# Performance work log

Measured on AMD Instinct MI355X. Metric: run time of the kernel, lower is better.

## Reference

```python
import jax, jax.numpy as jnp
import numpy as np

# constants mirroring init_kwargs
SPATIAL_STRIDE = 4
RADIUS2 = 0.5 ** 2
K = 32


def _fps(xyz, m):
    """Iterative farthest point sampling. xyz: [N,3] -> idx [m] int32 (starts at index 0, like pointnet2)."""
    n = xyz.shape[0]

    def body(i, carry):
        dist, idx = carry
        cur = xyz[idx[i]]                              # [3]
        d = jnp.sum((xyz - cur) ** 2, axis=-1)          # [N]
        dist = jnp.minimum(dist, d)
        idx = idx.at[i + 1].set(jnp.argmax(dist).astype(jnp.int32))
        return dist, idx

    dist0 = jnp.full((n,), 1e10, xyz.dtype)
    idx0 = jnp.zeros((m,), jnp.int32)
    _, idx = jax.lax.fori_loop(0, m - 1, body, (dist0, idx0))
    return idx


def setup_inputs() -> dict:
    key = jax.random.key(0)
    ks = jax.random.split(key, 5)
    B, T, N, C = 4, 8, 2048, 64
    C_IN = 2 * C + 3  # grouped feat2 + anchor feat1 + xyz displacement
    xyzs = jax.random.uniform(ks[0], (B, T, N, 3), dtype=jnp.float32)
    features = jax.random.normal(ks[1], (B, T, N, C), dtype=jnp.float32)
    w1 = jax.random.normal(ks[2], (C_IN, 128), dtype=jnp.float32) / np.sqrt(C_IN)
    w2 = jax.random.normal(ks[3], (128, 128), dtype=jnp.float32) / np.sqrt(128)
    w3 = jax.random.normal(ks[4], (128, 256), dtype=jnp.float32) / np.sqrt(128)
    return {
        "xyzs": xyzs, "features": features,
        "w1": w1, "b1": jnp.zeros((128,), jnp.float32),
        "w2": w2, "b2": jnp.zeros((128,), jnp.float32),
        "w3": w3, "b3": jnp.zeros((256,), jnp.float32),
    }


def reference(xyzs, features, w1, b1, w2, b2, w3, b3):
    B, T, N, _ = xyzs.shape
    M = N // SPATIAL_STRIDE

    # temporal replicate padding [1,1]
    xp = jnp.concatenate([xyzs[:, :1], xyzs, xyzs[:, -1:]], axis=1)        # [B,T+2,N,3]
    fp = jnp.concatenate([features[:, :1], features, features[:, -1:]], axis=1)
    # frames processed: i = 1..T (stride 1); neighbor frame = i+1
    xyz_a, xyz_n = xp[:, 1:T + 1], xp[:, 2:T + 2]                          # [B,T,N,3]
    feat_a, feat_n = fp[:, 1:T + 1], fp[:, 2:T + 2]                        # [B,T,N,C]

    gather = jax.vmap(jax.vmap(lambda a, i: a[i]))  # over (B, T)

    # FPS on each anchor frame
    idx = jax.vmap(jax.vmap(lambda p: _fps(p, M)))(xyz_a)                  # [B,T,M]
    anchor = gather(xyz_a, idx)                                            # [B,T,M,3]
    f1 = gather(feat_a, idx)                                               # [B,T,M,C]

    # knn of anchors into next frame, with ball-query radius clamp
    d = jnp.sum((anchor[:, :, :, None, :] - xyz_n[:, :, None, :, :]) ** 2, axis=-1)  # [B,T,M,N]
    negd, idxk = jax.lax.top_k(-d, K)                                      # [B,T,M,K]
    idxk = jnp.where(-negd <= RADIUS2, idxk, idxk[..., :1])                # duplicate nearest outside radius

    gxyz = gather(xyz_n, idxk)                                             # [B,T,M,K,3]
    gf2 = gather(feat_n, idxk)                                             # [B,T,M,K,C]
    disp = gxyz - anchor[:, :, :, None, :]
    h = jnp.concatenate(
        [gf2, jnp.broadcast_to(f1[:, :, :, None, :], gf2.shape), disp], axis=-1)  # [B,T,M,K,2C+3]

    h = jax.nn.relu(h @ w1 + b1)
    h = jax.nn.relu(h @ w2 + b2)
    h = jax.nn.relu(h @ w3 + b3)
    new_features = jnp.max(h, axis=3)                                      # [B,T,M,256]
    return anchor, new_features
```

## Files before the change

### kernel.cpp

```cpp
#include <hip/hip_runtime.h>

#define BB 4
#define TT 8
#define NN 2048
#define CC 64
#define MM 512
#define KK 32
#define H3DIM 256
#define RAD2 0.25f
#define FINF 3.4e38f

typedef _Float16 f16x8 __attribute__((ext_vector_type(8)));
typedef _Float16 f16x4 __attribute__((ext_vector_type(4)));
typedef float f32x4 __attribute__((ext_vector_type(4)));

template <int CTRL>
__device__ __forceinline__ float dpp_max_step(float x) {
    int xi = __builtin_bit_cast(int, x);
    int yi = __builtin_amdgcn_update_dpp(xi, xi, CTRL, 0xf, 0xf, false);
    return fmaxf(x, __builtin_bit_cast(float, yi));
}
__device__ __forceinline__ float wave_max64(float x) {
    x = dpp_max_step<0x111>(x);
    x = dpp_max_step<0x112>(x);
    x = dpp_max_step<0x114>(x);
    x = dpp_max_step<0x118>(x);
    x = dpp_max_step<0x142>(x);
    x = dpp_max_step<0x143>(x);
    return __builtin_bit_cast(float, __builtin_amdgcn_readlane(__builtin_bit_cast(int, x), 63));
}
template <int CTRL>
__device__ __forceinline__ unsigned long long dpp_minkey_step(unsigned long long k) {
    int lo = (int)(unsigned)k;
    int hi = (int)(unsigned)(k >> 32);
    int slo = __builtin_amdgcn_update_dpp(lo, lo, CTRL, 0xf, 0xf, false);
    int shi = __builtin_amdgcn_update_dpp(hi, hi, CTRL, 0xf, 0xf, false);
    unsigned long long s = ((unsigned long long)(unsigned)shi << 32) | (unsigned)slo;
    return s < k ? s : k;
}
__device__ __forceinline__ unsigned long long wave_minkey(unsigned long long k) {
    k = dpp_minkey_step<0x111>(k);
    k = dpp_minkey_step<0x112>(k);
    k = dpp_minkey_step<0x114>(k);
    k = dpp_minkey_step<0x118>(k);
    k = dpp_minkey_step<0x142>(k);
    k = dpp_minkey_step<0x143>(k);
    int lo = __builtin_amdgcn_readlane((int)(unsigned)k, 63);
    int hi = __builtin_amdgcn_readlane((int)(unsigned)(k >> 32), 63);
    return ((unsigned long long)(unsigned)hi << 32) | (unsigned)lo;
}

#define FPP_LDS 52224

__global__ __launch_bounds__(256) void k_fps_pp(const float* __restrict__ xyzs,
                                                const float* __restrict__ feats,
                                                const float* __restrict__ w1,
                                                int* __restrict__ fps_idx,
                                                _Float16* __restrict__ Pp) {
    extern __shared__ char fsm[];
    int tid = threadIdx.x;

    if (blockIdx.x < BB * TT) {
        float* sx = (float*)fsm;
        float* sy = sx + NN;
        float* sz = sy + NN;
        float* pd = sz + NN;
        int* pi = (int*)(pd + 8);
        int bt = blockIdx.x;
        int lane = tid & 63, w = tid >> 6;
        const float* src = xyzs + (size_t)bt * NN * 3;
        for (int i = tid; i < NN; i += 256) {
            sx[i] = src[i * 3 + 0];
            sy[i] = src[i * 3 + 1];
            sz[i] = src[i * 3 + 2];
        }
        __syncthreads();

        float px[8], py[8], pz[8], dist[8];
#pragma unroll
        for (int j = 0; j < 8; ++j) {
            int p = tid * 8 + j;
            px[j] = sx[p]; py[j] = sy[p]; pz[j] = sz[p];
            dist[j] = 1e10f;
        }

        int cur = 0;
        if (tid == 0) fps_idx[bt * MM + 0] = 0;
        int pbase = tid * 8;

        for (int it = 1; it < MM; ++it) {
            float cx = sx[cur], cy = sy[cur], cz = sz[cur];
            float bestd = -1.0f;
            int bestp = 0;
#pragma unroll
            for (int j = 0; j < 8; ++j) {
                float dx = px[j] - cx, dy = py[j] - cy, dz = pz[j] - cz;
                float d = dx * dx + dy * dy + dz * dz;
                float nd = fminf(dist[j], d);
                dist[j] = nd;
                if (nd > bestd) { bestd = nd; bestp = pbase + j; }
            }
            float wmax = wave_max64(bestd);
            unsigned long long mask = __ballot(bestd == wmax);
            int wl = __ffsll(mask) - 1;
            int wbp = __builtin_amdgcn_readlane(bestp, wl);
            if (lane == 0) { pd[(it & 1) * 4 + w] = wmax; pi[(it & 1) * 4 + w] = wbp; }
            __syncthreads();
            float bd = pd[(it & 1) * 4 + 0];
            int bp = pi[(it & 1) * 4 + 0];
#pragma unroll
            for (int q = 1; q < 4; ++q) {
                float d2 = pd[(it & 1) * 4 + q];
                int p2 = pi[(it & 1) * 4 + q];
                if (d2 > bd) { bd = d2; bp = p2; }
            }
            cur = bp;
            if (tid == 0) fps_idx[bt * MM + it] = cur;
        }
    } else {
        float* sw = (float*)fsm;
        float* sin_ = sw + 68 * 128;
        for (int i = tid; i < 68 * 128; i += 256) {
            int r = i >> 7, c = i & 127;
            float v = 0.f;
            if (r < 64) v = w1[r * 128 + c];
            else if (r < 67) v = w1[(128 + r - 64) * 128 + c];
            sw[i] = v;
        }
        int row0 = (blockIdx.x - BB * TT) * 64;
        int bt = row0 >> 11;
        int b = bt >> 3, t = bt & 7;
        int tn = (t + 1 < TT) ? (t + 1) : (TT - 1);
        size_t nbase = (size_t)(b * TT + tn) * NN + (row0 & (NN - 1));
        const float* fsrc = feats + nbase * CC;
        const float* xsrc = xyzs + nbase * 3;
        for (int i = tid; i < 1024; i += 256) {
            float4 v = ((const float4*)fsrc)[i];
            int r = i >> 4, c = (i & 15) * 4;
            *(float4*)&sin_[r * 68 + c] = v;
        }
        if (tid < 192) {
            int r = tid / 3, c = tid - r * 3;
            sin_[r * 68 + 64 + c] = xsrc[tid];
        }
        if (tid < 64) sin_[tid * 68 + 67] = 0.f;
        __syncthreads();

        int rowg = tid >> 5, colg = tid & 31;
        float4 acc[8];
#pragma unroll
        for (int i = 0; i < 8; ++i) acc[i] = make_float4(0.f, 0.f, 0.f, 0.f);
        for (int k = 0; k < 68; k += 4) {
            float4 a4[8], b4[4];
#pragma unroll
            for (int i = 0; i < 8; ++i) a4[i] = *(const float4*)&sin_[(rowg * 8 + i) * 68 + k];
#pragma unroll
            for (int kk = 0; kk < 4; ++kk) b4[kk] = *(const float4*)&sw[(k + kk) * 128 + colg * 4];
#pragma unroll
            for (int i = 0; i < 8; ++i) {
#pragma unroll
                for (int kk = 0; kk < 4; ++kk) {
                    float av = (kk == 0) ? a4[i].x : (kk == 1) ? a4[i].y : (kk == 2) ? a4[i].z : a4[i].w;
                    acc[i].x += av * b4[kk].x;
                    acc[i].y += av * b4[kk].y;
                    acc[i].z += av * b4[kk].z;
                    acc[i].w += av * b4[kk].w;
                }
            }
        }
#pragma unroll
        for (int i = 0; i < 8; ++i) {
            f16x4 h;
            h[0] = (_Float16)acc[i].x; h[1] = (_Float16)acc[i].y;
            h[2] = (_Float16)acc[i].z; h[3] = (_Float16)acc[i].w;
            *(f16x4*)&Pp[(size_t)(row0 + rowg * 8 + i) * 128 + colg * 4] = h;
        }
    }
}

__global__ __launch_bounds__(256) void k_knn(const float* __restrict__ xyzs,
                                             const int* __restrict__ fps_idx,
                                             int* __restrict__ idxk) {
    __shared__ float sx[NN], sy[NN], sz[NN];
    int tid = threadIdx.x;
    int wave = tid >> 6, lane = tid & 63;
    int bt = blockIdx.x >> 6;
    int sub = blockIdx.x & 63;
    int b = bt >> 3, t = bt & 7;
    int tn = (t + 1 < TT) ? (t + 1) : (TT - 1);
    const float* src = xyzs + ((size_t)(b * TT + tn)) * NN * 3;
    for (int i = tid; i < NN; i += 256) {
        sx[i] = src[i * 3 + 0];
        sy[i] = src[i * 3 + 1];
        sz[i] = src[i * 3 + 2];
    }
    __syncthreads();

    for (int a = 0; a < 2; ++a) {
        int mrow = bt * MM + sub * 8 + wave * 2 + a;
        int aidx = fps_idx[mrow];
        const float* xs = xyzs + ((size_t)bt * NN + aidx) * 3;
        float ax = xs[0], ay = xs[1], az = xs[2];
        float d[32];
#pragma unroll
        for (int j = 0; j < 32; ++j) {
            int p = j * 64 + lane;
            float dx = sx[p] - ax, dy = sy[p] - ay, dz = sz[p] - az;
            d[j] = dx * dx + dy * dy + dz * dz;
        }
        float gd[4];
        int gp[4];
#pragma unroll
        for (int g = 0; g < 4; ++g) {
            gd[g] = d[g * 8];
            gp[g] = (g * 8) * 64 + lane;
#pragma unroll
            for (int jj = 1; jj < 8; ++jj) {
                float dj = d[g * 8 + jj];
                if (dj < gd[g]) { gd[g] = dj; gp[g] = (g * 8 + jj) * 64 + lane; }
            }
        }

        int p0 = 0;
        int myidx = 0;
        for (int r = 0; r < KK; ++r) {
            bool u01 = gd[1] < gd[0], u23 = gd[3] < gd[2];
            float da = u01 ? gd[1] : gd[0], db = u23 ? gd[3] : gd[2];
            int pa = u01 ? gp[1] : gp[0], pb = u23 ? gp[3] : gp[2];
            bool uf = db < da;
            float bd = uf ? db : da;
            int bp = uf ? pb : pa;
            unsigned long long key =
                ((unsigned long long)(unsigned)__builtin_bit_cast(unsigned, bd) << 32) |
                (unsigned)bp;
            unsigned long long wkey = wave_minkey(key);
            int pstar = (int)(unsigned)wkey;
            float dstar = __builtin_bit_cast(float, (unsigned)(wkey >> 32));
            if (r == 0) { p0 = pstar; myidx = pstar; }
            int outp = (dstar <= RAD2) ? pstar : p0;
            if (lane == r) myidx = outp;
            if (r < KK - 1) {
                int lanew = pstar & 63;
                int jw = pstar >> 6;
                int gsel = jw >> 3;
                int jl = jw & 7;
                bool imw = (lane == lanew);
#define KNN_RECOMP(G)                                                         \
                {                                                             \
                    _Pragma("unroll")                                         \
                    for (int jj = 0; jj < 8; ++jj) {                          \
                        float dj = d[(G) * 8 + jj];                           \
                        dj = (imw && jj == jl) ? FINF : dj;                   \
                        d[(G) * 8 + jj] = dj;                                 \
                    }                                                         \
                    gd[G] = d[(G) * 8];                                       \
                    gp[G] = ((G) * 8) * 64 + lane;                            \
                    _Pragma("unroll")                                         \
                    for (int jj = 1; jj < 8; ++jj) {                          \
                        float dj = d[(G) * 8 + jj];                           \
                        if (dj < gd[G]) { gd[G] = dj; gp[G] = ((G) * 8 + jj) * 64 + lane; } \
                    }                                                         \
                }
                switch (gsel) {
                    case 0: KNN_RECOMP(0); break;
                    case 1: KNN_RECOMP(1); break;
                    case 2: KNN_RECOMP(2); break;
                    default: KNN_RECOMP(3); break;
                }
#undef KNN_RECOMP
            }
        }
        if (lane < KK) idxk[(size_t)mrow * KK + lane] = myidx;
    }
}

#define SM_W2 0
#define SM_W3 32768
#define SM_H1 98304
#define SM_H2 114688
#define SM_B2 131072
#define SM_B3 131584
#define SM_TOTAL 132608

__global__ __launch_bounds__(1024, 1) void k_mlp(const float* __restrict__ xyzs,
                                                 const float* __restrict__ feats,
                                                 const float* __restrict__ w1,
                                                 const float* __restrict__ b1,
                                                 const int* __restrict__ fps_idx,
                                                 const _Float16* __restrict__ Pp,
                                                 float* __restrict__ Qp,
                                                 const int* __restrict__ idxk,
                                                 const float* __restrict__ w2,
                                                 const float* __restrict__ b2,
                                                 const float* __restrict__ w3,
                                                 const float* __restrict__ b3,
                                                 float* __restrict__ out_anchor,
                                                 float* __restrict__ out_feat) {
    extern __shared__ char smem[];
    int tid = threadIdx.x;
    int bid = blockIdx.x;

    {
        float* qsw = (float*)smem;
        float* qsin = qsw + 68 * 128;
        float* qsb = qsin + 64 * 68;
        for (int i = tid; i < 68 * 128; i += 1024) {
            int r = i >> 7, c = i & 127;
            float v = 0.f;
            if (r < 64) v = w1[(64 + r) * 128 + c];
            else if (r < 67) v = w1[(128 + r - 64) * 128 + c];
            qsw[i] = v;
        }
        if (tid < 128) qsb[tid] = b1[tid];
        int row0 = bid * 64;
        int bt0 = row0 >> 9;
        size_t fbase = (size_t)bt0 * NN;
        {
            int r = tid >> 4, seg = tid & 15;
            int aidx = fps_idx[row0 + r];
            const float4* fr = (const float4*)(feats + (fbase + aidx) * CC);
            float4 v = fr[seg];
            *(float4*)&qsin[r * 68 + seg * 4] = v;
        }
        if (tid < 64) {
            int aidx = fps_idx[row0 + tid];
            const float* xs = xyzs + (fbase + aidx) * 3;
            float x = xs[0], y = xs[1], z = xs[2];
            qsin[tid * 68 + 64] = -x;
            qsin[tid * 68 + 65] = -y;
            qsin[tid * 68 + 66] = -z;
            qsin[tid * 68 + 67] = 0.f;
            out_anchor[(size_t)(row0 + tid) * 3 + 0] = x;
            out_anchor[(size_t)(row0 + tid) * 3 + 1] = y;
            out_anchor[(size_t)(row0 + tid) * 3 + 2] = z;
        }
        __syncthreads();

        int rowg = tid >> 5, colg = tid & 31;
        float4 bias = *(const float4*)&qsb[colg * 4];
        float4 acc[2];
#pragma unroll
        for (int i = 0; i < 2; ++i) acc[i] = bias;
        for (int k = 0; k < 68; k += 4) {
            float4 a4[2], b4[4];
#pragma unroll
            for (int i = 0; i < 2; ++i) a4[i] = *(const float4*)&qsin[(rowg * 2 + i) * 68 + k];
#pragma unroll
            for (int kk = 0; kk < 4; ++kk) b4[kk] = *(const float4*)&qsw[(k + kk) * 128 + colg * 4];
#pragma unroll
            for (int i = 0; i < 2; ++i) {
#pragma unroll
                for (int kk = 0; kk < 4; ++kk) {
                    float av = (kk == 0) ? a4[i].x : (kk == 1) ? a4[i].y : (kk == 2) ? a4[i].z : a4[i].w;
                    acc[i].x += av * b4[kk].x;
                    acc[i].y += av * b4[kk].y;
                    acc[i].z += av * b4[kk].z;
                    acc[i].w += av * b4[kk].w;
                }
            }
        }
#pragma unroll
        for (int i = 0; i < 2; ++i)
            *(float4*)&Qp[(size_t)(row0 + rowg * 2 + i) * 128 + colg * 4] = acc[i];
    }
    __syncthreads();

    for (int i = tid; i < 128 * 128; i += 1024) {
        int n = i & 127, kk = i >> 7;
        _Float16 v = (_Float16)w2[kk * 128 + n];
        *(_Float16*)(smem + SM_W2 + n * 256 + ((2 * kk) ^ ((n & 7) << 4))) = v;
    }
    for (int i = tid; i < 256 * 128; i += 1024) {
        int n = i & 255, kk = i >> 8;
        _Float16 v = (_Float16)w3[kk * 256 + n];
        *(_Float16*)(smem + SM_W3 + n * 256 + ((2 * kk) ^ ((n & 7) << 4))) = v;
    }
    if (tid < 128) *(float*)(smem + SM_B2 + tid * 4) = b2[tid];
    if (tid < 256) *(float*)(smem + SM_B3 + tid * 4) = b3[tid];
    __syncthreads();

    int lane = tid & 63;
    int w = tid >> 6;
    int wm = w >> 3, wn = w & 7;
    int l15 = lane & 15, g = lane >> 4;
    int hswz = (l15 & 7) << 4;

    const f32x4 zero4 = {0.f, 0.f, 0.f, 0.f};

    for (int c = 0; c < 32; ++c) {
        int a0 = bid * 64 + c * 2;
        int bt = a0 >> 9;

        {
            int r = tid >> 4, seg = tid & 15;
            int arow = a0 + (r >> 5);
            int kidx = r & 31;
            int nk = idxk[(size_t)arow * KK + kidx];
            const _Float16* ps = Pp + ((size_t)(bt * NN + nk)) * 128 + seg * 8;
            const float* qs = Qp + (size_t)arow * 128 + seg * 8;
            int rowbase = SM_H1 + r * 256;
            int swz = (r & 7) << 4;
            f16x8 pv = *(const f16x8*)ps;
            f32x4 q0 = *(const f32x4*)qs;
            f32x4 q1 = *(const f32x4*)(qs + 4);
            f16x8 hv;
#pragma unroll
            for (int j = 0; j < 4; ++j) hv[j] = (_Float16)fmaxf((float)pv[j] + q0[j], 0.f);
#pragma unroll
            for (int j = 0; j < 4; ++j) hv[4 + j] = (_Float16)fmaxf((float)pv[4 + j] + q1[j], 0.f);
            *(f16x8*)(smem + rowbase + ((seg * 16) ^ swz)) = hv;
        }
        __syncthreads();

        f32x4 acc2[2];
#pragma unroll
        for (int m = 0; m < 2; ++m) acc2[m] = zero4;

#pragma unroll
        for (int ks = 0; ks < 4; ++ks) {
            int kbyte = ks * 64 + g * 16;
            f16x8 af[2], bf;
#pragma unroll
            for (int m = 0; m < 2; ++m) {
                int row = wm * 32 + m * 16 + l15;
                af[m] = *(const f16x8*)(smem + SM_H1 + row * 256 + (kbyte ^ hswz));
            }
            {
                int col = wn * 16 + l15;
                bf = *(const f16x8*)(smem + SM_W2 + col * 256 + (kbyte ^ hswz));
            }
#pragma unroll
            for (int m = 0; m < 2; ++m)
                acc2[m] = __builtin_amdgcn_mfma_f32_16x16x32_f16(af[m], bf, acc2[m], 0, 0, 0);
        }
#pragma unroll
        for (int m = 0; m < 2; ++m) {
            int col = wn * 16 + l15;
            float bb = *(const float*)(smem + SM_B2 + col * 4);
#pragma unroll
            for (int r = 0; r < 4; ++r) {
                int row = wm * 32 + m * 16 + g * 4 + r;
                float v = fmaxf(acc2[m][r] + bb, 0.f);
                *(_Float16*)(smem + SM_H2 + row * 256 + ((2 * col) ^ ((row & 7) << 4))) = (_Float16)v;
            }
        }
        __syncthreads();

        f32x4 acc3[2][2];
#pragma unroll
        for (int m = 0; m < 2; ++m)
#pragma unroll
            for (int n = 0; n < 2; ++n) acc3[m][n] = zero4;

#pragma unroll
        for (int ks = 0; ks < 4; ++ks) {
            int kbyte = ks * 64 + g * 16;
            f16x8 af[2], bf[2];
#pragma unroll
            for (int m = 0; m < 2; ++m) {
                int row = wm * 32 + m * 16 + l15;
                af[m] = *(const f16x8*)(smem + SM_H2 + row * 256 + (kbyte ^ hswz));
            }
#pragma unroll
            for (int n = 0; n < 2; ++n) {
                int col = wn * 32 + n * 16 + l15;
                bf[n] = *(const f16x8*)(smem + SM_W3 + col * 256 + (kbyte ^ hswz));
            }
#pragma unroll
            for (int m = 0; m < 2; ++m)
#pragma unroll
                for (int n = 0; n < 2; ++n)
                    acc3[m][n] = __builtin_amdgcn_mfma_f32_16x16x32_f16(af[m], bf[n], acc3[m][n], 0, 0, 0);
        }
#pragma unroll
        for (int n = 0; n < 2; ++n) {
            int col = wn * 32 + n * 16 + l15;
            float s = acc3[0][n][0];
#pragma unroll
            for (int r = 1; r < 4; ++r) s = fmaxf(s, acc3[0][n][r]);
#pragma unroll
            for (int r = 0; r < 4; ++r) s = fmaxf(s, acc3[1][n][r]);
            s = fmaxf(s, __shfl_xor(s, 16));
            s = fmaxf(s, __shfl_xor(s, 32));
            if (g == 0) {
                float bb = *(const float*)(smem + SM_B3 + col * 4);
                out_feat[(size_t)(a0 + wm) * H3DIM + col] = fmaxf(s + bb, 0.f);
            }
        }
        __syncthreads();
    }
}

extern "C" void kernel_launch(void* const* d_in, const int* in_sizes, int n_in,
                              void* d_out, int out_size, void* d_ws, size_t ws_size,
                              hipStream_t stream) {
    const float* xyzs  = (const float*)d_in[0];
    const float* feats = (const float*)d_in[1];
    const float* w1 = (const float*)d_in[2];
    const float* b1 = (const float*)d_in[3];
    const float* w2 = (const float*)d_in[4];
    const float* b2 = (const float*)d_in[5];
    const float* w3 = (const float*)d_in[6];
    const float* b3 = (const float*)d_in[7];

    float* out_anchor = (float*)d_out;
    float* out_feat = out_anchor + (size_t)BB * TT * MM * 3;

    char* ws = (char*)d_ws;
    int* fps_idx = (int*)ws;
    int* idxk = (int*)(ws + 65536);
    _Float16* Pp = (_Float16*)(ws + 65536 + 2097152);
    float* Qp = (float*)(ws + 65536 + 2097152 + 16777216);
    if (ws_size < (size_t)(65536 + 2097152 + 16777216) + (size_t)BB * TT * MM * 128 * 4)
        return;

    (void)hipFuncSetAttribute((const void*)k_fps_pp, hipFuncAttributeMaxDynamicSharedMemorySize, FPP_LDS);
    k_fps_pp<<<BB * TT + BB * TT * NN / 64, 256, FPP_LDS, stream>>>(xyzs, feats, w1, fps_idx, Pp);
    k_knn<<<BB * TT * 64, 256, 0, stream>>>(xyzs, fps_idx, idxk);

    (void)hipFuncSetAttribute((const void*)k_mlp, hipFuncAttributeMaxDynamicSharedMemorySize, SM_TOTAL);
    k_mlp<<<256, 1024, SM_TOTAL, stream>>>(xyzs, feats, w1, b1, fps_idx, Pp, Qp, idxk,
                                           w2, b2, w3, b3, out_anchor, out_feat);
}
```

Measured before the change: 515.9 us.

## Fuse kNN selection into MLP kernel and keep neighbor indices in LDS

Removes the separate kNN kernel launch. The MLP kernel now computes the 32 nearest neighbors for its 64 anchors itself, after the Q projection, and stores the indices in shared memory instead of a global idxk buffer. This saves one launch, the global write and read of the indices, and the separate pass of loading xyz into LDS. In exchange, the kNN work now runs on only 256 blocks of 1024 threads (4 anchors per wave) rather than 2048 smaller blocks, which may lower parallelism for that phase. The Qp row index was also changed to bid*64, which appears to match the previous row0.

```diff
diff --git a/kernel.cpp b/kernel.cpp
--- a/kernel.cpp
+++ b/kernel.cpp
@@ -178,109 +178,14 @@
     }
 }
 
-__global__ __launch_bounds__(256) void k_knn(const float* __restrict__ xyzs,
-                                             const int* __restrict__ fps_idx,
-                                             int* __restrict__ idxk) {
-    __shared__ float sx[NN], sy[NN], sz[NN];
-    int tid = threadIdx.x;
-    int wave = tid >> 6, lane = tid & 63;
-    int bt = blockIdx.x >> 6;
-    int sub = blockIdx.x & 63;
-    int b = bt >> 3, t = bt & 7;
-    int tn = (t + 1 < TT) ? (t + 1) : (TT - 1);
-    const float* src = xyzs + ((size_t)(b * TT + tn)) * NN * 3;
-    for (int i = tid; i < NN; i += 256) {
-        sx[i] = src[i * 3 + 0];
-        sy[i] = src[i * 3 + 1];
-        sz[i] = src[i * 3 + 2];
-    }
-    __syncthreads();
-
-    for (int a = 0; a < 2; ++a) {
-        int mrow = bt * MM + sub * 8 + wave * 2 + a;
-        int aidx = fps_idx[mrow];
-        const float* xs = xyzs + ((size_t)bt * NN + aidx) * 3;
-        float ax = xs[0], ay = xs[1], az = xs[2];
-        float d[32];
-#pragma unroll
-        for (int j = 0; j < 32; ++j) {
-            int p = j * 64 + lane;
-            float dx = sx[p] - ax, dy = sy[p] - ay, dz = sz[p] - az;
-            d[j] = dx * dx + dy * dy + dz * dz;
-        }
-        float gd[4];
-        int gp[4];
-#pragma unroll
-        for (int g = 0; g < 4; ++g) {
-            gd[g] = d[g * 8];
-            gp[g] = (g * 8) * 64 + lane;
-#pragma unroll
-            for (int jj = 1; jj < 8; ++jj) {
-                float dj = d[g * 8 + jj];
-                if (dj < gd[g]) { gd[g] = dj; gp[g] = (g * 8 + jj) * 64 + lane; }
-            }
-        }
-
-        int p0 = 0;
-        int myidx = 0;
-        for (int r = 0; r < KK; ++r) {
-            bool u01 = gd[1] < gd[0], u23 = gd[3] < gd[2];
-            float da = u01 ? gd[1] : gd[0], db = u23 ? gd[3] : gd[2];
-            int pa = u01 ? gp[1] : gp[0], pb = u23 ? gp[3] : gp[2];
-            bool uf = db < da;
-            float bd = uf ? db : da;
-            int bp = uf ? pb : pa;
-            unsigned long long key =
-                ((unsigned long long)(unsigned)__builtin_bit_cast(unsigned, bd) << 32) |
-                (unsigned)bp;
-            unsigned long long wkey = wave_minkey(key);
-            int pstar = (int)(unsigned)wkey;
-            float dstar = __builtin_bit_cast(float, (unsigned)(wkey >> 32));
-            if (r == 0) { p0 = pstar; myidx = pstar; }
-            int outp = (dstar <= RAD2) ? pstar : p0;
-            if (lane == r) myidx = outp;
-            if (r < KK - 1) {
-                int lanew = pstar & 63;
-                int jw = pstar >> 6;
-                int gsel = jw >> 3;
-                int jl = jw & 7;
-                bool imw = (lane == lanew);
-#define KNN_RECOMP(G)                                                         \
-                {                                                             \
-                    _Pragma("unroll")                                         \
-                    for (int jj = 0; jj < 8; ++jj) {                          \
-                        float dj = d[(G) * 8 + jj];                           \
-                        dj = (imw && jj == jl) ? FINF : dj;                   \
-                        d[(G) * 8 + jj] = dj;                                 \
-                    }                                                         \
-                    gd[G] = d[(G) * 8];                                       \
-                    gp[G] = ((G) * 8) * 64 + lane;                            \
-                    _Pragma("unroll")                                         \
-                    for (int jj = 1; jj < 8; ++jj) {                          \
-                        float dj = d[(G) * 8 + jj];                           \
-                        if (dj < gd[G]) { gd[G] = dj; gp[G] = ((G) * 8 + jj) * 64 + lane; } \
-                    }                                                         \
-                }
-                switch (gsel) {
-                    case 0: KNN_RECOMP(0); break;
-                    case 1: KNN_RECOMP(1); break;
-                    case 2: KNN_RECOMP(2); break;
-                    default: KNN_RECOMP(3); break;
-                }
-#undef KNN_RECOMP
-            }
-        }
-        if (lane < KK) idxk[(size_t)mrow * KK + lane] = myidx;
-    }
-}
-
 #define SM_W2 0
 #define SM_W3 32768
 #define SM_H1 98304
 #define SM_H2 114688
 #define SM_B2 131072
 #define SM_B3 131584
-#define SM_TOTAL 132608
+#define SM_IDX 132608
+#define SM_TOTAL (132608 + 64 * KK * 4)
 
 __global__ __launch_bounds__(1024, 1) void k_mlp(const float* __restrict__ xyzs,
                                                  const float* __restrict__ feats,
@@ -289,7 +194,6 @@
                                                  const int* __restrict__ fps_idx,
                                                  const _Float16* __restrict__ Pp,
                                                  float* __restrict__ Qp,
-                                                 const int* __restrict__ idxk,
                                                  const float* __restrict__ w2,
                                                  const float* __restrict__ b2,
                                                  const float* __restrict__ w3,
@@ -299,6 +203,7 @@
     extern __shared__ char smem[];
     int tid = threadIdx.x;
     int bid = blockIdx.x;
+    int* sidx = (int*)(smem + SM_IDX);
 
     {
         float* qsw = (float*)smem;
@@ -361,7 +266,104 @@
         }
 #pragma unroll
         for (int i = 0; i < 2; ++i)
-            *(float4*)&Qp[(size_t)(row0 + rowg * 2 + i) * 128 + colg * 4] = acc[i];
+            *(float4*)&Qp[(size_t)(bid * 64 + rowg * 2 + i) * 128 + colg * 4] = acc[i];
+    }
+    __syncthreads();
+
+    {
+        float* sx = (float*)smem;
+        float* sy = sx + NN;
+        float* sz = sy + NN;
+        int row0 = bid * 64;
+        int bt = row0 >> 9;
+        int b = bt >> 3, t = bt & 7;
+        int tn = (t + 1 < TT) ? (t + 1) : (TT - 1);
+        const float* src = xyzs + ((size_t)(b * TT + tn)) * NN * 3;
+        for (int i = tid; i < NN; i += 1024) {
+            sx[i] = src[i * 3 + 0];
+            sy[i] = src[i * 3 + 1];
+            sz[i] = src[i * 3 + 2];
+        }
+        __syncthreads();
+
+        int wave = tid >> 6, lane = tid & 63;
+        for (int a = 0; a < 4; ++a) {
+            int la = wave * 4 + a;
+            int mrow = row0 + la;
+            int aidx = fps_idx[mrow];
+            const float* xs = xyzs + ((size_t)bt * NN + aidx) * 3;
+            float ax = xs[0], ay = xs[1], az = xs[2];
+            float d[32];
+#pragma unroll
+            for (int j = 0; j < 32; ++j) {
+                int p = j * 64 + lane;
+                float dx = sx[p] - ax, dy = sy[p] - ay, dz = sz[p] - az;
+                d[j] = dx * dx + dy * dy + dz * dz;
+            }
+            float gd[4];
+            int gp[4];
+#pragma unroll
+            for (int g = 0; g < 4; ++g) {
+                gd[g] = d[g * 8];
+                gp[g] = (g * 8) * 64 + lane;
+#pragma unroll
+                for (int jj = 1; jj < 8; ++jj) {
+                    float dj = d[g * 8 + jj];
+                    if (dj < gd[g]) { gd[g] = dj; gp[g] = (g * 8 + jj) * 64 + lane; }
+                }
+            }
+
+            int p0 = 0;
+            int myidx = 0;
+            for (int r = 0; r < KK; ++r) {
+                bool u01 = gd[1] < gd[0], u23 = gd[3] < gd[2];
+                float da = u01 ? gd[1] : gd[0], db = u23 ? gd[3] : gd[2];
+                int pa = u01 ? gp[1] : gp[0], pb = u23 ? gp[3] : gp[2];
+                bool uf = db < da;
+                float bd = uf ? db : da;
+                int bp = uf ? pb : pa;
+                unsigned long long key =
+                    ((unsigned long long)(unsigned)__builtin_bit_cast(unsigned, bd) << 32) |
+                    (unsigned)bp;
+                unsigned long long wkey = wave_minkey(key);
+                int pstar = (int)(unsigned)wkey;
+                float dstar = __builtin_bit_cast(float, (unsigned)(wkey >> 32));
+                if (r == 0) { p0 = pstar; myidx = pstar; }
+                int outp = (dstar <= RAD2) ? pstar : p0;
+                if (lane == r) myidx = outp;
+                if (r < KK - 1) {
+                    int lanew = pstar & 63;
+                    int jw = pstar >> 6;
+                    int gsel = jw >> 3;
+                    int jl = jw & 7;
+                    bool imw = (lane == lanew);
+#define KNN_RECOMP(G)                                                         \
+                    {                                                         \
+                        _Pragma("unroll")                                     \
+                        for (int jj = 0; jj < 8; ++jj) {                      \
+                            float dj = d[(G) * 8 + jj];                       \
+                            dj = (imw && jj == jl) ? FINF : dj;               \
+                            d[(G) * 8 + jj] = dj;                             \
+                        }                                                     \
+                        gd[G] = d[(G) * 8];                                   \
+                        gp[G] = ((G) * 8) * 64 + lane;                        \
+                        _Pragma("unroll")                                     \
+                        for (int jj = 1; jj < 8; ++jj) {                      \
+                            float dj = d[(G) * 8 + jj];                       \
+                            if (dj < gd[G]) { gd[G] = dj; gp[G] = ((G) * 8 + jj) * 64 + lane; } \
+                        }                                                     \
+                    }
+                    switch (gsel) {
+                        case 0: KNN_RECOMP(0); break;
+                        case 1: KNN_RECOMP(1); break;
+                        case 2: KNN_RECOMP(2); break;
+                        default: KNN_RECOMP(3); break;
+                    }
+#undef KNN_RECOMP
+                }
+            }
+            if (lane < KK) sidx[la * KK + lane] = myidx;
+        }
     }
     __syncthreads();
 
@@ -393,11 +395,11 @@
 
         {
             int r = tid >> 4, seg = tid & 15;
-            int arow = a0 + (r >> 5);
+            int la = c * 2 + (r >> 5);
             int kidx = r & 31;
-            int nk = idxk[(size_t)arow * KK + kidx];
+            int nk = sidx[la * KK + kidx];
             const _Float16* ps = Pp + ((size_t)(bt * NN + nk)) * 128 + seg * 8;
-            const float* qs = Qp + (size_t)arow * 128 + seg * 8;
+            const float* qs = Qp + (size_t)(bid * 64 + la) * 128 + seg * 8;
             int rowbase = SM_H1 + r * 256;
             int swz = (r & 7) << 4;
             f16x8 pv = *(const f16x8*)ps;
@@ -508,7 +510,6 @@
 
     char* ws = (char*)d_ws;
     int* fps_idx = (int*)ws;
-    int* idxk = (int*)(ws + 65536);
     _Float16* Pp = (_Float16*)(ws + 65536 + 2097152);
     float* Qp = (float*)(ws + 65536 + 2097152 + 16777216);
     if (ws_size < (size_t)(65536 + 2097152 + 16777216) + (size_t)BB * TT * MM * 128 * 4)
@@ -516,9 +517,8 @@
 
     (void)hipFuncSetAttribute((const void*)k_fps_pp, hipFuncAttributeMaxDynamicSharedMemorySize, FPP_LDS);
     k_fps_pp<<<BB * TT + BB * TT * NN / 64, 256, FPP_LDS, stream>>>(xyzs, feats, w1, fps_idx, Pp);
-    k_knn<<<BB * TT * 64, 256, 0, stream>>>(xyzs, fps_idx, idxk);
 
     (void)hipFuncSetAttribute((const void*)k_mlp, hipFuncAttributeMaxDynamicSharedMemorySize, SM_TOTAL);
-    k_mlp<<<256, 1024, SM_TOTAL, stream>>>(xyzs, feats, w1, b1, fps_idx, Pp, Qp, idxk,
+    k_mlp<<<256, 1024, SM_TOTAL, stream>>>(xyzs, feats, w1, b1, fps_idx, Pp, Qp,
                                            w2, b2, w3, b3, out_anchor, out_feat);
 }
```

Result: no change. 515.1 us (-0.1%).

## Halve MLP block size with larger per-wave MFMA tiles and XCD-aware block remap

Applied to the files above, without the earlier changes.

The MLP kernel now runs 512 threads per block instead of 1024. Each wave computes a wider output tile: 2x2 MFMA tiles for layer 2 and 2x4 for layer 3, so each A fragment loaded from shared memory is reused across more columns. Block indices are permuted so that blocks landing on the same XCD handle consecutive anchor rows, which share frames and should improve L2 locality for the Pp/Qp gathers. The trade-off is fewer waves per block to hide latency and more accumulator registers per wave.

```diff
diff --git a/kernel.cpp b/kernel.cpp
--- a/kernel.cpp
+++ b/kernel.cpp
@@ -282,29 +282,30 @@
 #define SM_B3 131584
 #define SM_TOTAL 132608
 
-__global__ __launch_bounds__(1024, 1) void k_mlp(const float* __restrict__ xyzs,
-                                                 const float* __restrict__ feats,
-                                                 const float* __restrict__ w1,
-                                                 const float* __restrict__ b1,
-                                                 const int* __restrict__ fps_idx,
-                                                 const _Float16* __restrict__ Pp,
-                                                 float* __restrict__ Qp,
-                                                 const int* __restrict__ idxk,
-                                                 const float* __restrict__ w2,
-                                                 const float* __restrict__ b2,
-                                                 const float* __restrict__ w3,
-                                                 const float* __restrict__ b3,
-                                                 float* __restrict__ out_anchor,
-                                                 float* __restrict__ out_feat) {
+__global__ __launch_bounds__(512)
+void k_mlp(const float* __restrict__ xyzs,
+           const float* __restrict__ feats,
+           const float* __restrict__ w1,
+           const float* __restrict__ b1,
+           const int* __restrict__ fps_idx,
+           const _Float16* __restrict__ Pp,
+           float* __restrict__ Qp,
+           const int* __restrict__ idxk,
+           const float* __restrict__ w2,
+           const float* __restrict__ b2,
+           const float* __restrict__ w3,
+           const float* __restrict__ b3,
+           float* __restrict__ out_anchor,
+           float* __restrict__ out_feat) {
     extern __shared__ char smem[];
     int tid = threadIdx.x;
-    int bid = blockIdx.x;
+    int bid = ((blockIdx.x & 7) << 5) | (blockIdx.x >> 3);
 
     {
         float* qsw = (float*)smem;
         float* qsin = qsw + 68 * 128;
         float* qsb = qsin + 64 * 68;
-        for (int i = tid; i < 68 * 128; i += 1024) {
+        for (int i = tid; i < 68 * 128; i += 512) {
             int r = i >> 7, c = i & 127;
             float v = 0.f;
             if (r < 64) v = w1[(64 + r) * 128 + c];
@@ -316,11 +317,14 @@
         int bt0 = row0 >> 9;
         size_t fbase = (size_t)bt0 * NN;
         {
-            int r = tid >> 4, seg = tid & 15;
+            int r = tid >> 3, seg = tid & 7;
             int aidx = fps_idx[row0 + r];
             const float4* fr = (const float4*)(feats + (fbase + aidx) * CC);
-            float4 v = fr[seg];
-            *(float4*)&qsin[r * 68 + seg * 4] = v;
+#pragma unroll
+            for (int i = 0; i < 2; ++i) {
+                float4 v = fr[seg * 2 + i];
+                *(float4*)&qsin[r * 68 + (seg * 2 + i) * 4] = v;
+            }
         }
         if (tid < 64) {
             int aidx = fps_idx[row0 + tid];
@@ -338,17 +342,17 @@
 
         int rowg = tid >> 5, colg = tid & 31;
         float4 bias = *(const float4*)&qsb[colg * 4];
-        float4 acc[2];
-#pragma unroll
-        for (int i = 0; i < 2; ++i) acc[i] = bias;
+        float4 acc[4];
+#pragma unroll
+        for (int i = 0; i < 4; ++i) acc[i] = bias;
         for (int k = 0; k < 68; k += 4) {
-            float4 a4[2], b4[4];
-#pragma unroll
-            for (int i = 0; i < 2; ++i) a4[i] = *(const float4*)&qsin[(rowg * 2 + i) * 68 + k];
+            float4 a4[4], b4[4];
+#pragma unroll
+            for (int i = 0; i < 4; ++i) a4[i] = *(const float4*)&qsin[(rowg * 4 + i) * 68 + k];
 #pragma unroll
             for (int kk = 0; kk < 4; ++kk) b4[kk] = *(const float4*)&qsw[(k + kk) * 128 + colg * 4];
 #pragma unroll
-            for (int i = 0; i < 2; ++i) {
+            for (int i = 0; i < 4; ++i) {
 #pragma unroll
                 for (int kk = 0; kk < 4; ++kk) {
                     float av = (kk == 0) ? a4[i].x : (kk == 1) ? a4[i].y : (kk == 2) ? a4[i].z : a4[i].w;
@@ -360,17 +364,17 @@
             }
         }
 #pragma unroll
-        for (int i = 0; i < 2; ++i)
-            *(float4*)&Qp[(size_t)(row0 + rowg * 2 + i) * 128 + colg * 4] = acc[i];
+        for (int i = 0; i < 4; ++i)
+            *(float4*)&Qp[(size_t)(bid * 64 + rowg * 4 + i) * 128 + colg * 4] = acc[i];
     }
     __syncthreads();
 
-    for (int i = tid; i < 128 * 128; i += 1024) {
+    for (int i = tid; i < 128 * 128; i += 512) {
         int n = i & 127, kk = i >> 7;
         _Float16 v = (_Float16)w2[kk * 128 + n];
         *(_Float16*)(smem + SM_W2 + n * 256 + ((2 * kk) ^ ((n & 7) << 4))) = v;
     }
-    for (int i = tid; i < 256 * 128; i += 1024) {
+    for (int i = tid; i < 256 * 128; i += 512) {
         int n = i & 255, kk = i >> 8;
         _Float16 v = (_Float16)w3[kk * 256 + n];
         *(_Float16*)(smem + SM_W3 + n * 256 + ((2 * kk) ^ ((n & 7) << 4))) = v;
@@ -381,7 +385,7 @@
 
     int lane = tid & 63;
     int w = tid >> 6;
-    int wm = w >> 3, wn = w & 7;
+    int wm = w >> 2, wn = w & 3;
     int l15 = lane & 15, g = lane >> 4;
     int hswz = (l15 & 7) << 4;
 
@@ -392,89 +396,99 @@
         int bt = a0 >> 9;
 
         {
-            int r = tid >> 4, seg = tid & 15;
+            int r = tid >> 3, seg = tid & 7;
             int arow = a0 + (r >> 5);
             int kidx = r & 31;
             int nk = idxk[(size_t)arow * KK + kidx];
-            const _Float16* ps = Pp + ((size_t)(bt * NN + nk)) * 128 + seg * 8;
-            const float* qs = Qp + (size_t)arow * 128 + seg * 8;
+            const _Float16* ps = Pp + ((size_t)(bt * NN + nk)) * 128 + seg * 16;
+            const float* qs = Qp + (size_t)arow * 128 + seg * 16;
             int rowbase = SM_H1 + r * 256;
             int swz = (r & 7) << 4;
-            f16x8 pv = *(const f16x8*)ps;
-            f32x4 q0 = *(const f32x4*)qs;
-            f32x4 q1 = *(const f32x4*)(qs + 4);
-            f16x8 hv;
-#pragma unroll
-            for (int j = 0; j < 4; ++j) hv[j] = (_Float16)fmaxf((float)pv[j] + q0[j], 0.f);
-#pragma unroll
-            for (int j = 0; j < 4; ++j) hv[4 + j] = (_Float16)fmaxf((float)pv[4 + j] + q1[j], 0.f);
-            *(f16x8*)(smem + rowbase + ((seg * 16) ^ swz)) = hv;
+#pragma unroll
+            for (int i = 0; i < 2; ++i) {
+                f16x8 pv = *(const f16x8*)(ps + i * 8);
+                f32x4 q0 = *(const f32x4*)(qs + i * 8);
+                f32x4 q1 = *(const f32x4*)(qs + i * 8 + 4);
+                f16x8 hv;
+#pragma unroll
+                for (int j = 0; j < 4; ++j) hv[j] = (_Float16)fmaxf((float)pv[j] + q0[j], 0.f);
+#pragma unroll
+                for (int j = 0; j < 4; ++j) hv[4 + j] = (_Float16)fmaxf((float)pv[4 + j] + q1[j], 0.f);
+                *(f16x8*)(smem + rowbase + ((seg * 32 + i * 16) ^ swz)) = hv;
+            }
         }
         __syncthreads();
 
-        f32x4 acc2[2];
-#pragma unroll
-        for (int m = 0; m < 2; ++m) acc2[m] = zero4;
+        f32x4 acc2[2][2];
+#pragma unroll
+        for (int m = 0; m < 2; ++m)
+#pragma unroll
+            for (int n = 0; n < 2; ++n) acc2[m][n] = zero4;
 
 #pragma unroll
         for (int ks = 0; ks < 4; ++ks) {
             int kbyte = ks * 64 + g * 16;
-            f16x8 af[2], bf;
+            f16x8 af[2], bf[2];
 #pragma unroll
             for (int m = 0; m < 2; ++m) {
                 int row = wm * 32 + m * 16 + l15;
                 af[m] = *(const f16x8*)(smem + SM_H1 + row * 256 + (kbyte ^ hswz));
             }
-            {
-                int col = wn * 16 + l15;
-                bf = *(const f16x8*)(smem + SM_W2 + col * 256 + (kbyte ^ hswz));
+#pragma unroll
+            for (int n = 0; n < 2; ++n) {
+                int col = wn * 32 + n * 16 + l15;
+                bf[n] = *(const f16x8*)(smem + SM_W2 + col * 256 + (kbyte ^ hswz));
             }
 #pragma unroll
             for (int m = 0; m < 2; ++m)
-                acc2[m] = __builtin_amdgcn_mfma_f32_16x16x32_f16(af[m], bf, acc2[m], 0, 0, 0);
-        }
-#pragma unroll
-        for (int m = 0; m < 2; ++m) {
-            int col = wn * 16 + l15;
-            float bb = *(const float*)(smem + SM_B2 + col * 4);
-#pragma unroll
-            for (int r = 0; r < 4; ++r) {
-                int row = wm * 32 + m * 16 + g * 4 + r;
-                float v = fmaxf(acc2[m][r] + bb, 0.f);
-                *(_Float16*)(smem + SM_H2 + row * 256 + ((2 * col) ^ ((row & 7) << 4))) = (_Float16)v;
-            }
-        }
+#pragma unroll
+                for (int n = 0; n < 2; ++n)
+                    acc2[m][n] = __builtin_amdgcn_mfma_f32_16x16x32_f16(af[m], bf[n], acc2[m][n], 0, 0, 0);
+        }
+#pragma unroll
+        for (int m = 0; m < 2; ++m)
+#pragma unroll
+            for (int n = 0; n < 2; ++n) {
+                int col = wn * 32 + n * 16 + l15;
+                float bb = *(const float*)(smem + SM_B2 + col * 4);
+#pragma unroll
+                for (int r = 0; r < 4; ++r) {
+                    int row = wm * 32 + m * 16 + g * 4 + r;
+                    float v = fmaxf(acc2[m][n][r] + bb, 0.f);
+                    *(_Float16*)(smem + SM_H2 + row * 256 + ((2 * col) ^ ((row & 7) << 4))) = (_Float16)v;
+                }
+            }
         __syncthreads();
 
-        f32x4 acc3[2][2];
+        f32x4 acc3[2][4];
 #pragma unroll
         for (int m = 0; m < 2; ++m)
 #pragma unroll
-            for (int n = 0; n < 2; ++n) acc3[m][n] = zero4;
+            for (int n = 0; n < 4; ++n) acc3[m][n] = zero4;
 
 #pragma unroll
         for (int ks = 0; ks < 4; ++ks) {
             int kbyte = ks * 64 + g * 16;
-            f16x8 af[2], bf[2];
+            f16x8 af[2], bf[4];
 #pragma unroll
             for (int m = 0; m < 2; ++m) {
                 int row = wm * 32 + m * 16 + l15;
                 af[m] = *(const f16x8*)(smem + SM_H2 + row * 256 + (kbyte ^ hswz));
             }
 #pragma unroll
-            for (int n = 0; n < 2; ++n) {
-                int col = wn * 32 + n * 16 + l15;
+            for (int n = 0; n < 4; ++n) {
+                int col = wn * 64 + n * 16 + l15;
                 bf[n] = *(const f16x8*)(smem + SM_W3 + col * 256 + (kbyte ^ hswz));
             }
 #pragma unroll
             for (int m = 0; m < 2; ++m)
 #pragma unroll
-                for (int n = 0; n < 2; ++n)
+                for (int n = 0; n < 4; ++n)
                     acc3[m][n] = __builtin_amdgcn_mfma_f32_16x16x32_f16(af[m], bf[n], acc3[m][n], 0, 0, 0);
         }
 #pragma unroll
-        for (int n = 0; n < 2; ++n) {
-            int col = wn * 32 + n * 16 + l15;
+        for (int n = 0; n < 4; ++n) {
+            int col = wn * 64 + n * 16 + l15;
             float s = acc3[0][n][0];
 #pragma unroll
             for (int r = 1; r < 4; ++r) s = fmaxf(s, acc3[0][n][r]);
@@ -519,6 +533,6 @@
     k_knn<<<BB * TT * 64, 256, 0, stream>>>(xyzs, fps_idx, idxk);
 
     (void)hipFuncSetAttribute((const void*)k_mlp, hipFuncAttributeMaxDynamicSharedMemorySize, SM_TOTAL);
-    k_mlp<<<256, 1024, SM_TOTAL, stream>>>(xyzs, feats, w1, b1, fps_idx, Pp, Qp, idxk,
-                                           w2, b2, w3, b3, out_anchor, out_feat);
-}
+    k_mlp<<<256, 512, SM_TOTAL, stream>>>(xyzs, feats, w1, b1, fps_idx, Pp, Qp, idxk,
+                                          w2, b2, w3, b3, out_anchor, out_feat);
+}
```

New measurement: 519.0 us. No clear change (+0.6%).
